# Optimization experiments

Measured on AMD Instinct MI355X. Metric: run time of the kernel, lower is better.

## Reference

```python
import jax, jax.numpy as jnp
import numpy as np

B, S, V, E, H = 4096, 64, 100000, 128, 128

_PARAM_NAMES = ["Wz", "Uzl", "Uzr", "Wr", "Url", "Urr", "Wh", "Uhl", "Uhr"]


def setup_inputs() -> dict:
    key = jax.random.key(0)
    ks = jax.random.split(key, 2 + 2 * len(_PARAM_NAMES))
    inp = {"tokens": jax.random.randint(ks[0], (B, S), 0, V)}
    inp["emb"] = jax.random.normal(ks[1], (V, E), jnp.float32)
    i = 2
    for n in _PARAM_NAMES:
        din = E if n.startswith("W") else H
        inp[n] = jax.random.normal(ks[i], (din, H), jnp.float32) / np.sqrt(din).astype(np.float32)
        i += 1
        inp["b" + n] = jax.random.normal(ks[i], (H,), jnp.float32) * 0.01
        i += 1
    return inp


def _tree_gru(word, hl, hr, p):
    # word: [..., E], hl/hr: [..., H]
    z = jax.nn.sigmoid(word @ p["Wz"] + p["bWz"] + hl @ p["Uzl"] + p["bUzl"] + hr @ p["Uzr"] + p["bUzr"])
    r = jax.nn.sigmoid(word @ p["Wr"] + p["bWr"] + hl @ p["Url"] + p["bUrl"] + hr @ p["Urr"] + p["bUrr"])
    h_tilde = jnp.tanh(word @ p["Wh"] + p["bWh"] + (r * hl) @ p["Uhl"] + p["bUhl"] + (r * hr) @ p["Uhr"] + p["bUhr"])
    return z * hl + z * hr + (1.0 - z) * h_tilde


def reference(tokens, emb, Wz, bWz, Uzl, bUzl, Uzr, bUzr, Wr, bWr, Url, bUrl, Urr, bUrr, Wh, bWh, Uhl, bUhl, Uhr, bUhr):
    p = dict(Wz=Wz, bWz=bWz, Uzl=Uzl, bUzl=bUzl, Uzr=Uzr, bUzr=bUzr,
             Wr=Wr, bWr=bWr, Url=Url, bUrl=bUrl, Urr=Urr, bUrr=bUrr,
             Wh=Wh, bWh=bWh, Uhl=Uhl, bUhl=bUhl, Uhr=Uhr, bUhr=bUhr)
    x = emb[tokens]                                   # [B, S, E]
    h0 = jnp.zeros(x.shape[:2] + (H,), x.dtype)
    cur = _tree_gru(x, h0, h0, p)                     # leaf nodes [B, S, H]
    n = cur.shape[1]
    while n > 1:                                      # static loop over log2(S) tree levels
        left, right = cur[:, 0::2], cur[:, 1::2]      # pair adjacent nodes
        word0 = jnp.zeros(left.shape[:2] + (E,), cur.dtype)
        cur = _tree_gru(word0, left, right, p)
        n //= 2
    return cur.transpose(1, 0, 2)                     # [1, B, H] (matches torch transpose(0,1))
```

## Files before the change

kernel.cpp:

```cpp
#include <hip/hip_runtime.h>


typedef _Float16 half_t;
typedef __attribute__((ext_vector_type(2))) _Float16 f16x2;
typedef __attribute__((ext_vector_type(8))) _Float16 f16x8;
typedef __attribute__((ext_vector_type(4))) float f32x4;

#define NTOK 262144
#define NB 4096
#define NV 100000

__device__ __forceinline__ float sigm(float x){
  float e = __expf(-x);
  return __builtin_amdgcn_rcpf(1.0f + e);
}
__device__ __forceinline__ float tanh_(float x){
  float e = __expf(2.f*x);
  float r = __builtin_amdgcn_rcpf(1.0f + e);
  return __builtin_fmaf(-2.0f, r, 1.0f);
}

__global__ __launch_bounds__(256) void wprep_k(
    const float* Wz, const float* Wh,
    const float* Uzl,const float* Uzr,const float* Url,const float* Urr,
    const float* Uhl,const float* Uhr,
    const float* bWz,const float* bUzl,const float* bUzr,
    const float* bWr,const float* bUrl,const float* bUrr,
    const float* bWh,const float* bUhl,const float* bUhr,
    half_t* wb, float* bc){
  int idx = blockIdx.x*256 + threadIdx.x;
  if (idx < 32768){
    const float* W = (idx < 16384) ? Wz : Wh;
    int t = idx & 16383;
    int w = t >> 11, ks = (t >> 9) & 3, l = (t >> 3) & 63, j = t & 7;
    int n = w*16 + (l & 15);
    int k = ks*32 + ((l >> 4) << 3) + j;
    wb[idx] = (half_t)W[k*128 + n];
  } else {
    int t = idx - 32768;
    int mat = t >> 15;
    t &= 32767;
    int w = t >> 12, ks = (t >> 9) & 7, l = (t >> 3) & 63, j = t & 7;
    int n = w*16 + (l & 15);
    int kp = ks*32 + ((l >> 4) << 3) + j;
    int k = kp >> 1;
    const float* U;
    if (mat == 0) U = (kp & 1) ? Uzr : Uzl;
    else if (mat == 1) U = (kp & 1) ? Urr : Url;
    else U = (kp & 1) ? Uhr : Uhl;
    wb[idx] = (half_t)U[k*128 + n];
  }
  if (blockIdx.x == 511 && threadIdx.x < 128){
    int j = threadIdx.x;
    bc[j]       = bWz[j] + bUzl[j] + bUzr[j];
    bc[128 + j] = bWr[j] + bUrl[j] + bUrr[j];
    bc[256 + j] = bWh[j] + bUhl[j] + bUhr[j];
  }
}

template<int MT>
__global__ __launch_bounds__(512, 8) void h1tab_k(
    const float* __restrict__ emb,
    const half_t* __restrict__ Wz_f, const half_t* __restrict__ Wh_f,
    const float* __restrict__ bc, half_t* __restrict__ t1)
{
  __shared__ __align__(16) _Float16 xs[MT*16][136];
  const int tid = threadIdx.x;
  const int m0  = blockIdx.x*(MT*16);
  #pragma unroll
  for (int it = 0; it < MT; it++){
    int idx = it*512 + tid;
    int m = idx >> 5, c = idx & 31;
    int row = m0 + m; if (row >= NV) row = 0;
    float4 v = ((const float4*)(emb + (size_t)row*128))[c];
    union { half_t h[4]; ushort4 u; } p;
    p.h[0]=(half_t)v.x; p.h[1]=(half_t)v.y; p.h[2]=(half_t)v.z; p.h[3]=(half_t)v.w;
    *(ushort4*)&xs[m][c*4] = p.u;
  }
  __syncthreads();
  const int w = tid>>6, l = tid&63;
  const int lr = l&15, lk = (l>>4)*8, lq = (l>>4)*4;
  const int col = w*16 + lr;

  f32x4 zacc[MT] = {}; f32x4 hacc[MT] = {};
  const half_t* wzp = Wz_f + ((w*4)*64 + l)*8;
  const half_t* whp = Wh_f + ((w*4)*64 + l)*8;
  #pragma unroll
  for (int ks=0; ks<4; ks++){
    f16x8 bz = *(const f16x8*)(wzp + ks*512);
    f16x8 bh = *(const f16x8*)(whp + ks*512);
    #pragma unroll
    for (int mt=0; mt<MT; mt++){
      f16x8 a = *(const f16x8*)&xs[mt*16 + lr][ks*32 + lk];
      zacc[mt] = __builtin_amdgcn_mfma_f32_16x16x32_f16(a, bz, zacc[mt],0,0,0);
      hacc[mt] = __builtin_amdgcn_mfma_f32_16x16x32_f16(a, bh, hacc[mt],0,0,0);
    }
  }
  const float bzv = bc[col], bhv = bc[256+col];
  #pragma unroll
  for (int mt=0; mt<MT; mt++){
    #pragma unroll
    for (int q=0; q<4; q++){
      int row = m0 + mt*16 + lq + q;
      if (row < NV){
        float z  = sigm(zacc[mt][q] + bzv);
        float ht = tanh_(hacc[mt][q] + bhv);
        t1[(size_t)row*128 + col] = (half_t)((1.f-z)*ht);
      }
    }
  }
}

template<int MT>
__global__ __launch_bounds__(512, 4) void tree1_k(
    const half_t* __restrict__ hin, const int* __restrict__ tokens,
    half_t* __restrict__ hout,
    const half_t* __restrict__ Uz_f, const half_t* __restrict__ Ur_f, const half_t* __restrict__ Uh_f,
    const float* __restrict__ bc)
{
  __shared__ __align__(16) _Float16 xs[MT*16][264];
  const int tid = threadIdx.x;
  const int m0  = blockIdx.x*(MT*16);
  #pragma unroll
  for (int it = 0; it < MT; it++){
    int idx = it*512 + tid;
    int m = idx >> 5, c = idx & 31;
    int tl = tokens[2*(m0+m)], tr = tokens[2*(m0+m)+1];
    uint2 A  = *(const uint2*)(hin + (size_t)tl*128 + c*4);
    uint2 Bv = *(const uint2*)(hin + (size_t)tr*128 + c*4);
    uint4 o;
    o.x = (A.x & 0xFFFFu) | (Bv.x << 16);
    o.y = (A.x >> 16)     | (Bv.x & 0xFFFF0000u);
    o.z = (A.y & 0xFFFFu) | (Bv.y << 16);
    o.w = (A.y >> 16)     | (Bv.y & 0xFFFF0000u);
    *(uint4*)&xs[m][c*8] = o;
  }
  __syncthreads();
  const int w = tid>>6, l = tid&63;
  const int lr = l&15, lk = (l>>4)*8, lq = (l>>4)*4;
  const int col = w*16 + lr;

  f32x4 zacc[MT] = {}, racc[MT] = {};
  const half_t* uzp = Uz_f + ((w*8)*64 + l)*8;
  const half_t* urp = Ur_f + ((w*8)*64 + l)*8;
  f16x8 bz_n = *(const f16x8*)uzp;
  f16x8 br_n = *(const f16x8*)urp;
  #pragma unroll
  for (int ks=0; ks<8; ks++){
    f16x8 bz = bz_n, br = br_n;
    if (ks < 7){
      bz_n = *(const f16x8*)(uzp + (ks+1)*512);
      br_n = *(const f16x8*)(urp + (ks+1)*512);
    }
    #pragma unroll
    for (int mt=0; mt<MT; mt++){
      f16x8 a = *(const f16x8*)&xs[mt*16 + lr][ks*32 + lk];
      zacc[mt] = __builtin_amdgcn_mfma_f32_16x16x32_f16(a, bz, zacc[mt],0,0,0);
      racc[mt] = __builtin_amdgcn_mfma_f32_16x16x32_f16(a, br, racc[mt],0,0,0);
    }
  }
  __syncthreads();

  uint zp[MT][2], sp[MT][2];
  const float bzv = bc[col], brv = bc[128+col];
  #pragma unroll
  for (int mt=0; mt<MT; mt++){
    union { half_t h[4]; uint u[2]; } pz, ps;
    #pragma unroll
    for (int q=0; q<4; q++){
      int row = mt*16 + lq + q;
      union { uint u; half_t h[2]; } io;
      io.u = *(uint*)&xs[row][2*col];
      float hl = (float)io.h[0];
      float hr = (float)io.h[1];
      float z  = sigm(zacc[mt][q] + bzv);
      float rv = sigm(racc[mt][q] + brv);
      pz.h[q] = (half_t)z;
      ps.h[q] = (half_t)(hl + hr);
      io.h[0] = (half_t)(rv*hl);
      io.h[1] = (half_t)(rv*hr);
      *(uint*)&xs[row][2*col] = io.u;
    }
    zp[mt][0]=pz.u[0]; zp[mt][1]=pz.u[1];
    sp[mt][0]=ps.u[0]; sp[mt][1]=ps.u[1];
  }
  __syncthreads();

  f32x4 ha[MT] = {};
  const half_t* uhp = Uh_f + ((w*8)*64 + l)*8;
  f16x8 bh_n = *(const f16x8*)uhp;
  #pragma unroll
  for (int ks=0; ks<8; ks++){
    f16x8 bh = bh_n;
    if (ks < 7) bh_n = *(const f16x8*)(uhp + (ks+1)*512);
    #pragma unroll
    for (int mt=0; mt<MT; mt++){
      f16x8 a = *(const f16x8*)&xs[mt*16 + lr][ks*32 + lk];
      ha[mt] = __builtin_amdgcn_mfma_f32_16x16x32_f16(a, bh, ha[mt],0,0,0);
    }
  }
  const float bhv = bc[256+col];
  #pragma unroll
  for (int mt=0; mt<MT; mt++){
    union { half_t h[4]; uint u[2]; } pz, ps;
    pz.u[0]=zp[mt][0]; pz.u[1]=zp[mt][1];
    ps.u[0]=sp[mt][0]; ps.u[1]=sp[mt][1];
    #pragma unroll
    for (int q=0; q<4; q++){
      int row = mt*16 + lq + q;
      float ht = tanh_(ha[mt][q] + bhv);
      float z  = (float)pz.h[q];
      float o  = z*(float)ps.h[q] + (1.f-z)*ht;
      hout[(size_t)(m0+row)*128 + col] = (half_t)o;
    }
  }
}

template<int MT, int RV, int LAST>
static __device__ __forceinline__ void level_step(
    _Float16 (*X)[264], _Float16 (*Y)[264], int tid,
    const half_t* Uz_f, const half_t* Ur_f, const half_t* Uh_f,
    const float* bc, float* outf, int outrow0)
{
  const int w = tid>>6, l = tid&63;
  const int lr = l&15, lk = (l>>4)*8, lq = (l>>4)*4;
  const int col = w*16 + lr;

  f32x4 zacc[MT] = {}, racc[MT] = {};
  const half_t* uzp = Uz_f + ((w*8)*64 + l)*8;
  const half_t* urp = Ur_f + ((w*8)*64 + l)*8;
  #pragma unroll
  for (int ks=0; ks<8; ks++){
    f16x8 bz = *(const f16x8*)(uzp + ks*512);
    f16x8 br = *(const f16x8*)(urp + ks*512);
    #pragma unroll
    for (int mt=0; mt<MT; mt++){
      f16x8 a = *(const f16x8*)&X[mt*16 + lr][ks*32 + lk];
      zacc[mt] = __builtin_amdgcn_mfma_f32_16x16x32_f16(a, bz, zacc[mt],0,0,0);
      racc[mt] = __builtin_amdgcn_mfma_f32_16x16x32_f16(a, br, racc[mt],0,0,0);
    }
  }
  __syncthreads();

  uint zp[MT][2], sp[MT][2];
  const float bzv = bc[col], brv = bc[128+col];
  #pragma unroll
  for (int mt=0; mt<MT; mt++){
    union { half_t h[4]; uint u[2]; } pz, ps;
    #pragma unroll
    for (int q=0; q<4; q++){
      int row = mt*16 + lq + q;
      union { uint u; half_t h[2]; } io;
      io.u = *(uint*)&X[row][2*col];
      float hl = (float)io.h[0];
      float hr = (float)io.h[1];
      float z  = sigm(zacc[mt][q] + bzv);
      float rv = sigm(racc[mt][q] + brv);
      pz.h[q] = (half_t)z;
      ps.h[q] = (half_t)(hl + hr);
      io.h[0] = (half_t)(rv*hl);
      io.h[1] = (half_t)(rv*hr);
      *(uint*)&X[row][2*col] = io.u;
    }
    zp[mt][0]=pz.u[0]; zp[mt][1]=pz.u[1];
    sp[mt][0]=ps.u[0]; sp[mt][1]=ps.u[1];
  }
  __syncthreads();

  f32x4 ha[MT] = {};
  const half_t* uhp = Uh_f + ((w*8)*64 + l)*8;
  #pragma unroll
  for (int ks=0; ks<8; ks++){
    f16x8 bh = *(const f16x8*)(uhp + ks*512);
    #pragma unroll
    for (int mt=0; mt<MT; mt++){
      f16x8 a = *(const f16x8*)&X[mt*16 + lr][ks*32 + lk];
      ha[mt] = __builtin_amdgcn_mfma_f32_16x16x32_f16(a, bh, ha[mt],0,0,0);
    }
  }
  const float bhv = bc[256+col];
  #pragma unroll
  for (int mt=0; mt<MT; mt++){
    union { half_t h[4]; uint u[2]; } pz, ps;
    pz.u[0]=zp[mt][0]; pz.u[1]=zp[mt][1];
    ps.u[0]=sp[mt][0]; ps.u[1]=sp[mt][1];
    #pragma unroll
    for (int q=0; q<4; q++){
      int row = mt*16 + lq + q;
      if (row < RV){
        float ht = tanh_(ha[mt][q] + bhv);
        float z  = (float)pz.h[q];
        float o  = z*(float)ps.h[q] + (1.f-z)*ht;
        if (LAST) outf[(size_t)(outrow0 + row)*128 + col] = o;
        else      Y[row>>1][2*col + (row&1)] = (half_t)o;
      }
    }
  }
  __syncthreads();
}

__global__ __launch_bounds__(512, 6) void tree_tail_k(
    const half_t* __restrict__ hA, float* __restrict__ outf,
    const half_t* __restrict__ Uz_f, const half_t* __restrict__ Ur_f, const half_t* __restrict__ Uh_f,
    const float* __restrict__ bc)
{
  __shared__ __align__(16) _Float16 XA[64][264];
  __shared__ __align__(16) _Float16 XB[32][264];
  const int tid = threadIdx.x;
  const int g = blockIdx.x;
  #pragma unroll
  for (int it = 0; it < 4; it++){
    int idx = it*512 + tid;
    int m = idx >> 5, c = idx & 31;
    int b = m >> 4, i = m & 15;
    size_t base = ((size_t)(128*g + b*32 + 2*i))*128 + c*4;
    uint2 A  = *(const uint2*)(hA + base);
    uint2 Bv = *(const uint2*)(hA + base + 128);
    uint4 o;
    o.x = (A.x & 0xFFFFu) | (Bv.x << 16);
    o.y = (A.x >> 16)     | (Bv.x & 0xFFFF0000u);
    o.z = (A.y & 0xFFFFu) | (Bv.y << 16);
    o.w = (A.y >> 16)     | (Bv.y & 0xFFFF0000u);
    *(uint4*)&XA[m][c*8] = o;
  }
  __syncthreads();
  level_step<4,64,0>(XA, XB, tid, Uz_f, Ur_f, Uh_f, bc, outf, 0);
  level_step<2,32,0>(XB, XA, tid, Uz_f, Ur_f, Uh_f, bc, outf, 0);
  level_step<1,16,0>(XA, XB, tid, Uz_f, Ur_f, Uh_f, bc, outf, 0);
  level_step<1, 8,0>(XB, XA, tid, Uz_f, Ur_f, Uh_f, bc, outf, 0);
  level_step<1, 4,1>(XA, XB, tid, Uz_f, Ur_f, Uh_f, bc, outf, 4*g);
}

extern "C" void kernel_launch(void* const* d_in, const int* in_sizes, int n_in,
                              void* d_out, int out_size, void* d_ws, size_t ws_size,
                              hipStream_t stream) {
  const int*   tokens = (const int*)  d_in[0];
  const float* emb    = (const float*)d_in[1];
  const float* Wz  = (const float*)d_in[2];  const float* bWz  = (const float*)d_in[3];
  const float* Uzl = (const float*)d_in[4];  const float* bUzl = (const float*)d_in[5];
  const float* Uzr = (const float*)d_in[6];  const float* bUzr = (const float*)d_in[7];
  const float* Wr  = (const float*)d_in[8];  const float* bWr  = (const float*)d_in[9];
  const float* Url = (const float*)d_in[10]; const float* bUrl = (const float*)d_in[11];
  const float* Urr = (const float*)d_in[12]; const float* bUrr = (const float*)d_in[13];
  const float* Wh  = (const float*)d_in[14]; const float* bWh  = (const float*)d_in[15];
  const float* Uhl = (const float*)d_in[16]; const float* bUhl = (const float*)d_in[17];
  const float* Uhr = (const float*)d_in[18]; const float* bUhr = (const float*)d_in[19];

  float*  bc = (float*)d_ws;
  half_t* wb = (half_t*)((char*)d_ws + 4096);
  half_t* Wz_f = wb;
  half_t* Wh_f = wb + 16384;
  half_t* Uz_f = wb + 32768;
  half_t* Ur_f = wb + 65536;
  half_t* Uh_f = wb + 98304;
  half_t* t1 = (half_t*)((char*)d_ws + (1<<20));
  half_t* hA = t1 + (size_t)NV*128;

  wprep_k<<<512, 256, 0, stream>>>(Wz,Wh,Uzl,Uzr,Url,Urr,Uhl,Uhr,
                                   bWz,bUzl,bUzr,bWr,bUrl,bUrr,bWh,bUhl,bUhr, wb, bc);

  h1tab_k<4><<<(NV + 63)/64, 512, 0, stream>>>(emb, Wz_f, Wh_f, bc, t1);

  tree1_k<8><<<(NTOK/2)/128, 512, 0, stream>>>(t1, tokens, hA, Uz_f, Ur_f, Uh_f, bc);

  tree_tail_k<<<1024, 512, 0, stream>>>(hA, (float*)d_out, Uz_f, Ur_f, Uh_f, bc);
}
```

Measured before the change: 135.8 us.

## Fuse first tree level into tail kernel, dropping intermediate global buffer

Removes the separate tree1 kernel and its global hA intermediate. Each tail block now gathers leaf pairs from the token table itself, runs the first level in two 64-row chunks into a larger shared buffer, then runs the remaining levels. This saves one launch and the global write and re-read of the level-1 states. In exchange the block uses more LDS, occupancy is capped at 2 blocks per CU, and there are only 1024 blocks, which may leave the first level less parallel and less able to hide gather latency.

```diff
diff --git a/kernel.cpp b/kernel.cpp
--- a/kernel.cpp
+++ b/kernel.cpp
@@ -2,7 +2,6 @@
 
 
 typedef _Float16 half_t;
-typedef __attribute__((ext_vector_type(2))) _Float16 f16x2;
 typedef __attribute__((ext_vector_type(8))) _Float16 f16x8;
 typedef __attribute__((ext_vector_type(4))) float f32x4;
 
@@ -111,116 +110,11 @@
   }
 }
 
-template<int MT>
-__global__ __launch_bounds__(512, 4) void tree1_k(
-    const half_t* __restrict__ hin, const int* __restrict__ tokens,
-    half_t* __restrict__ hout,
-    const half_t* __restrict__ Uz_f, const half_t* __restrict__ Ur_f, const half_t* __restrict__ Uh_f,
-    const float* __restrict__ bc)
-{
-  __shared__ __align__(16) _Float16 xs[MT*16][264];
-  const int tid = threadIdx.x;
-  const int m0  = blockIdx.x*(MT*16);
-  #pragma unroll
-  for (int it = 0; it < MT; it++){
-    int idx = it*512 + tid;
-    int m = idx >> 5, c = idx & 31;
-    int tl = tokens[2*(m0+m)], tr = tokens[2*(m0+m)+1];
-    uint2 A  = *(const uint2*)(hin + (size_t)tl*128 + c*4);
-    uint2 Bv = *(const uint2*)(hin + (size_t)tr*128 + c*4);
-    uint4 o;
-    o.x = (A.x & 0xFFFFu) | (Bv.x << 16);
-    o.y = (A.x >> 16)     | (Bv.x & 0xFFFF0000u);
-    o.z = (A.y & 0xFFFFu) | (Bv.y << 16);
-    o.w = (A.y >> 16)     | (Bv.y & 0xFFFF0000u);
-    *(uint4*)&xs[m][c*8] = o;
-  }
-  __syncthreads();
-  const int w = tid>>6, l = tid&63;
-  const int lr = l&15, lk = (l>>4)*8, lq = (l>>4)*4;
-  const int col = w*16 + lr;
-
-  f32x4 zacc[MT] = {}, racc[MT] = {};
-  const half_t* uzp = Uz_f + ((w*8)*64 + l)*8;
-  const half_t* urp = Ur_f + ((w*8)*64 + l)*8;
-  f16x8 bz_n = *(const f16x8*)uzp;
-  f16x8 br_n = *(const f16x8*)urp;
-  #pragma unroll
-  for (int ks=0; ks<8; ks++){
-    f16x8 bz = bz_n, br = br_n;
-    if (ks < 7){
-      bz_n = *(const f16x8*)(uzp + (ks+1)*512);
-      br_n = *(const f16x8*)(urp + (ks+1)*512);
-    }
-    #pragma unroll
-    for (int mt=0; mt<MT; mt++){
-      f16x8 a = *(const f16x8*)&xs[mt*16 + lr][ks*32 + lk];
-      zacc[mt] = __builtin_amdgcn_mfma_f32_16x16x32_f16(a, bz, zacc[mt],0,0,0);
-      racc[mt] = __builtin_amdgcn_mfma_f32_16x16x32_f16(a, br, racc[mt],0,0,0);
-    }
-  }
-  __syncthreads();
-
-  uint zp[MT][2], sp[MT][2];
-  const float bzv = bc[col], brv = bc[128+col];
-  #pragma unroll
-  for (int mt=0; mt<MT; mt++){
-    union { half_t h[4]; uint u[2]; } pz, ps;
-    #pragma unroll
-    for (int q=0; q<4; q++){
-      int row = mt*16 + lq + q;
-      union { uint u; half_t h[2]; } io;
-      io.u = *(uint*)&xs[row][2*col];
-      float hl = (float)io.h[0];
-      float hr = (float)io.h[1];
-      float z  = sigm(zacc[mt][q] + bzv);
-      float rv = sigm(racc[mt][q] + brv);
-      pz.h[q] = (half_t)z;
-      ps.h[q] = (half_t)(hl + hr);
-      io.h[0] = (half_t)(rv*hl);
-      io.h[1] = (half_t)(rv*hr);
-      *(uint*)&xs[row][2*col] = io.u;
-    }
-    zp[mt][0]=pz.u[0]; zp[mt][1]=pz.u[1];
-    sp[mt][0]=ps.u[0]; sp[mt][1]=ps.u[1];
-  }
-  __syncthreads();
-
-  f32x4 ha[MT] = {};
-  const half_t* uhp = Uh_f + ((w*8)*64 + l)*8;
-  f16x8 bh_n = *(const f16x8*)uhp;
-  #pragma unroll
-  for (int ks=0; ks<8; ks++){
-    f16x8 bh = bh_n;
-    if (ks < 7) bh_n = *(const f16x8*)(uhp + (ks+1)*512);
-    #pragma unroll
-    for (int mt=0; mt<MT; mt++){
-      f16x8 a = *(const f16x8*)&xs[mt*16 + lr][ks*32 + lk];
-      ha[mt] = __builtin_amdgcn_mfma_f32_16x16x32_f16(a, bh, ha[mt],0,0,0);
-    }
-  }
-  const float bhv = bc[256+col];
-  #pragma unroll
-  for (int mt=0; mt<MT; mt++){
-    union { half_t h[4]; uint u[2]; } pz, ps;
-    pz.u[0]=zp[mt][0]; pz.u[1]=zp[mt][1];
-    ps.u[0]=sp[mt][0]; ps.u[1]=sp[mt][1];
-    #pragma unroll
-    for (int q=0; q<4; q++){
-      int row = mt*16 + lq + q;
-      float ht = tanh_(ha[mt][q] + bhv);
-      float z  = (float)pz.h[q];
-      float o  = z*(float)ps.h[q] + (1.f-z)*ht;
-      hout[(size_t)(m0+row)*128 + col] = (half_t)o;
-    }
-  }
-}
-
 template<int MT, int RV, int LAST>
 static __device__ __forceinline__ void level_step(
     _Float16 (*X)[264], _Float16 (*Y)[264], int tid,
     const half_t* Uz_f, const half_t* Ur_f, const half_t* Uh_f,
-    const float* bc, float* outf, int outrow0)
+    const float* bc, float* outf, int outrow0, int slot0)
 {
   const int w = tid>>6, l = tid&63;
   const int lr = l&15, lk = (l>>4)*8, lq = (l>>4)*4;
@@ -292,43 +186,50 @@
         float z  = (float)pz.h[q];
         float o  = z*(float)ps.h[q] + (1.f-z)*ht;
         if (LAST) outf[(size_t)(outrow0 + row)*128 + col] = o;
-        else      Y[row>>1][2*col + (row&1)] = (half_t)o;
+        else      Y[slot0 + (row>>1)][2*col + (row&1)] = (half_t)o;
       }
     }
   }
   __syncthreads();
 }
 
-__global__ __launch_bounds__(512, 6) void tree_tail_k(
-    const half_t* __restrict__ hA, float* __restrict__ outf,
+__global__ __launch_bounds__(512, 2) void fused_k(
+    const half_t* __restrict__ t1, const int* __restrict__ tokens,
+    float* __restrict__ outf,
     const half_t* __restrict__ Uz_f, const half_t* __restrict__ Ur_f, const half_t* __restrict__ Uh_f,
     const float* __restrict__ bc)
 {
   __shared__ __align__(16) _Float16 XA[64][264];
-  __shared__ __align__(16) _Float16 XB[32][264];
+  __shared__ __align__(16) _Float16 XB[64][264];
   const int tid = threadIdx.x;
   const int g = blockIdx.x;
-  #pragma unroll
-  for (int it = 0; it < 4; it++){
-    int idx = it*512 + tid;
-    int m = idx >> 5, c = idx & 31;
-    int b = m >> 4, i = m & 15;
-    size_t base = ((size_t)(128*g + b*32 + 2*i))*128 + c*4;
-    uint2 A  = *(const uint2*)(hA + base);
-    uint2 Bv = *(const uint2*)(hA + base + 128);
-    uint4 o;
-    o.x = (A.x & 0xFFFFu) | (Bv.x << 16);
-    o.y = (A.x >> 16)     | (Bv.x & 0xFFFF0000u);
-    o.z = (A.y & 0xFFFFu) | (Bv.y << 16);
-    o.w = (A.y >> 16)     | (Bv.y & 0xFFFF0000u);
-    *(uint4*)&XA[m][c*8] = o;
-  }
-  __syncthreads();
-  level_step<4,64,0>(XA, XB, tid, Uz_f, Ur_f, Uh_f, bc, outf, 0);
-  level_step<2,32,0>(XB, XA, tid, Uz_f, Ur_f, Uh_f, bc, outf, 0);
-  level_step<1,16,0>(XA, XB, tid, Uz_f, Ur_f, Uh_f, bc, outf, 0);
-  level_step<1, 8,0>(XB, XA, tid, Uz_f, Ur_f, Uh_f, bc, outf, 0);
-  level_step<1, 4,1>(XA, XB, tid, Uz_f, Ur_f, Uh_f, bc, outf, 4*g);
+
+  #pragma unroll
+  for (int k = 0; k < 2; k++){
+    #pragma unroll
+    for (int it = 0; it < 4; it++){
+      int idx = it*512 + tid;
+      int m = idx >> 5, c = idx & 31;
+      int gm = 128*g + 64*k + m;
+      int tl = tokens[2*gm], tr = tokens[2*gm+1];
+      uint2 A  = *(const uint2*)(t1 + (size_t)tl*128 + c*4);
+      uint2 Bv = *(const uint2*)(t1 + (size_t)tr*128 + c*4);
+      uint4 o;
+      o.x = (A.x & 0xFFFFu) | (Bv.x << 16);
+      o.y = (A.x >> 16)     | (Bv.x & 0xFFFF0000u);
+      o.z = (A.y & 0xFFFFu) | (Bv.y << 16);
+      o.w = (A.y >> 16)     | (Bv.y & 0xFFFF0000u);
+      *(uint4*)&XA[m][c*8] = o;
+    }
+    __syncthreads();
+    level_step<4,64,0>(XA, XB, tid, Uz_f, Ur_f, Uh_f, bc, outf, 0, 32*k);
+  }
+
+  level_step<4,64,0>(XB, XA, tid, Uz_f, Ur_f, Uh_f, bc, outf, 0, 0);
+  level_step<2,32,0>(XA, XB, tid, Uz_f, Ur_f, Uh_f, bc, outf, 0, 0);
+  level_step<1,16,0>(XB, XA, tid, Uz_f, Ur_f, Uh_f, bc, outf, 0, 0);
+  level_step<1, 8,0>(XA, XB, tid, Uz_f, Ur_f, Uh_f, bc, outf, 0, 0);
+  level_step<1, 4,1>(XB, XA, tid, Uz_f, Ur_f, Uh_f, bc, outf, 4*g, 0);
 }
 
 extern "C" void kernel_launch(void* const* d_in, const int* in_sizes, int n_in,
@@ -354,14 +255,11 @@
   half_t* Ur_f = wb + 65536;
   half_t* Uh_f = wb + 98304;
   half_t* t1 = (half_t*)((char*)d_ws + (1<<20));
-  half_t* hA = t1 + (size_t)NV*128;
 
   wprep_k<<<512, 256, 0, stream>>>(Wz,Wh,Uzl,Uzr,Url,Urr,Uhl,Uhr,
                                    bWz,bUzl,bUzr,bWr,bUrl,bUrr,bWh,bUhl,bUhr, wb, bc);
 
   h1tab_k<4><<<(NV + 63)/64, 512, 0, stream>>>(emb, Wz_f, Wh_f, bc, t1);
 
-  tree1_k<8><<<(NTOK/2)/128, 512, 0, stream>>>(t1, tokens, hA, Uz_f, Ur_f, Uh_f, bc);
-
-  tree_tail_k<<<1024, 512, 0, stream>>>(hA, (float*)d_out, Uz_f, Ur_f, Uh_f, bc);
-}
+  fused_k<<<1024, 512, 0, stream>>>(t1, tokens, (float*)d_out, Uz_f, Ur_f, Uh_f, bc);
+}
```

Measured after the change: 133.7 us. Within noise of the previous version (-1.5%).
